# Performance work log

Measured on AMD Instinct MI355X. Metric: run time of the kernel, lower is better.

## Reference

```python
import jax, jax.numpy as jnp
import numpy as np

N_NODES = 20000
N_EDGES = 320000
N_INPUT = 128
N_HIDDEN = 128
N_LAYERS = 3
N_OUT = 2
C_WEIGHT = 1.0
BN_EPS = 1e-5


def _psi(z):
    # sign(z) * log(1 + |z|), the LorentzNet scalar map
    return jnp.sign(z) * jnp.log1p(jnp.abs(z))


def _mink_dot(a, b):
    # Minkowski inner product, metric diag(+1, -1, ..., -1)
    return a[:, 0] * b[:, 0] - jnp.sum(a[:, 1:] * b[:, 1:], axis=1)


def setup_inputs() -> dict:
    key = jax.random.key(0)
    ks = jax.random.split(key, 12)
    n, h, L = N_INPUT, N_HIDDEN, N_LAYERS
    d_in = 2 * n + 6
    f32 = jnp.float32
    inp = {
        "x": jax.random.normal(ks[0], (N_NODES, n), f32),
        "edge_index": jax.random.randint(ks[1], (2, N_EDGES), 0, N_NODES),
        "edge_attr": jax.random.normal(ks[2], (N_EDGES, 4), f32),
        # phi_e: Linear(d_in->h, no bias), BN(h), ReLU, Linear(h->h), ReLU
        "W1": (jax.random.normal(ks[3], (L, d_in, h), f32) / np.sqrt(d_in)).astype(f32),
        "gamma": jnp.ones((L, h), f32),
        "beta": jnp.zeros((L, h), f32),
        "W2": (jax.random.normal(ks[4], (L, h, h), f32) / np.sqrt(h)).astype(f32),
        "b2": jnp.zeros((L, h), f32),
        # phi_x: Linear(h->h), ReLU, Linear(h->1, no bias, xavier gain 1e-3)
        "Wa": (jax.random.normal(ks[5], (L, h, h), f32) / np.sqrt(h)).astype(f32),
        "ba": jnp.zeros((L, h), f32),
        "Wb": (jax.random.normal(ks[6], (L, h, 1), f32) * 1e-3).astype(f32),
        # phi_m: Linear(h->1), Sigmoid
        "Wm": (jax.random.normal(ks[7], (L, h, 1), f32) / np.sqrt(h)).astype(f32),
        "bm": jnp.zeros((L, 1), f32),
        # final edge_mlp: Linear(h -> N_OUT)
        "We": (jax.random.normal(ks[8], (h, N_OUT), f32) / np.sqrt(h)).astype(f32),
        "be": jnp.zeros((N_OUT,), f32),
    }
    return inp


def _lgeb_layer(x, row, col, edge_attr, W1, gamma, beta, W2, b2, Wa, ba, Wb, Wm, bm):
    x_i = x[row]                       # [E, n] gather (aggregation target)
    x_j = x[col]                       # [E, n]
    x_diff = x_i - x_j                 # [E, n]
    norms = _psi(_mink_dot(x_diff, x_diff))[:, None]   # [E, 1]
    dots = _psi(_mink_dot(x_i, x_j))[:, None]          # [E, 1]
    m = jnp.concatenate([x_i, x_j, edge_attr, norms, dots], axis=1)  # [E, 2n+6]
    # phi_e
    hpre = m @ W1                                       # [E, h]
    mu = jnp.mean(hpre, axis=0)
    var = jnp.mean(jnp.square(hpre - mu), axis=0)       # biased, torch BN train mode
    hbn = (hpre - mu) * jax.lax.rsqrt(var + BN_EPS) * gamma + beta
    hid = jax.nn.relu(hbn)
    m_ij = jax.nn.relu(hid @ W2 + b2)                   # [E, h]
    # phi_m gate
    w = jax.nn.sigmoid(m_ij @ Wm + bm)                  # [E, 1]
    m_ij = m_ij * w
    # phi_x scalar weight on x_diff
    s = jax.nn.relu(m_ij @ Wa + ba) @ Wb                # [E, 1]
    trans = jnp.clip(x_diff * s, -100.0, 100.0)         # [E, n]
    x_agg = jax.ops.segment_sum(trans, row, num_segments=x.shape[0])  # [N, n]
    return x + C_WEIGHT * x_agg


def reference(x, edge_index, edge_attr, W1, gamma, beta, W2, b2,
              Wa, ba, Wb, Wm, bm, We, be):
    row, col = edge_index[0], edge_index[1]
    for l in range(N_LAYERS):
        x = _lgeb_layer(x, row, col, edge_attr,
                        W1[l], gamma[l], beta[l], W2[l], b2[l],
                        Wa[l], ba[l], Wb[l], Wm[l], bm[l])
    return jax.nn.sigmoid(x @ We + be)                  # [N, N_OUT]


if __name__ == "__main__":
    out = reference(**setup_inputs())
    print(out.shape, out.dtype)
```

## Files before the change

kernel.cpp:

```cpp
#include <hip/hip_runtime.h>
#include <math.h>

#define NND 20000
#define NE  320000
#define NF  128
#define EPS 1e-5f
#define TE  64
#define NT  256
#define NTILES (NE / TE)
#define NGRP (NE / 4)
#define XST 136
#define BST 40

typedef short short8 __attribute__((ext_vector_type(8)));
typedef float float4v __attribute__((ext_vector_type(4)));

__device__ __forceinline__ float psif(float z) {
    return copysignf(log1pf(fabsf(z)), z);
}
__device__ __forceinline__ float sigm(float z) {
    return 1.f / (1.f + expf(-z));
}
__device__ __forceinline__ short f2bf(float f) {
    union { float f; unsigned u; } v; v.f = f;
    unsigned r = v.u + 0x7fffu + ((v.u >> 16) & 1u);
    return (short)(r >> 16);
}
__device__ __forceinline__ float bf2f(short u) {
    union { unsigned u; float f; } v; v.u = ((unsigned)(unsigned short)u) << 16;
    return v.f;
}
__device__ __forceinline__ float clipf(float v) {
    return fminf(fmaxf(v, -100.f), 100.f);
}

__device__ __forceinline__ void stage_b(const unsigned short* __restrict__ wsrc, int wstride,
                                        int ks, short* bt, int t) {
    #pragma unroll
    for (int rr = 0; rr < 2; ++rr) {
        int c = t + rr * 256;
        int n = c >> 2, h = c & 3;
        short8 v = *(const short8*)(wsrc + (size_t)n * wstride + ks * 32 + h * 8);
        *(short8*)(bt + n * BST + h * 8) = v;
    }
}

__device__ __forceinline__ void ldreg_b(const unsigned short* __restrict__ w, int wstride,
                                        int ks, int t, short8* r) {
    #pragma unroll
    for (int rr = 0; rr < 2; ++rr) {
        int c = t + rr * 256;
        int n = c >> 2, h = c & 3;
        r[rr] = *(const short8*)(w + (size_t)n * wstride + ks * 32 + h * 8);
    }
}
__device__ __forceinline__ void wrlds_b(short* bt, int t, const short8* r) {
    #pragma unroll
    for (int rr = 0; rr < 2; ++rr) {
        int c = t + rr * 256;
        int n = c >> 2, h = c & 3;
        *(short8*)(bt + n * BST + h * 8) = r[rr];
    }
}

__global__ __launch_bounds__(NT, 2)
void node_gemm(const float* __restrict__ x,
               const unsigned short* __restrict__ wt,
               float* __restrict__ PQ,
               float* __restrict__ gstats)
{
    __shared__ short lxa[TE * XST];
    __shared__ short lbt[128 * BST];

    const int t = threadIdx.x;
    const int lane = t & 63, quad = lane >> 4, ln15 = lane & 15;
    const int wv = t >> 6, we = wv >> 1, wc = wv & 1;
    const int n0 = blockIdx.x * 64;
    const int ch = blockIdx.y;
    const unsigned short* wsrc = wt + (size_t)ch * 128 * 128;

    if (blockIdx.x == 0 && ch == 0) gstats[t] = 0.f;

    {
        int row = t >> 2, q = t & 3;
        int src = min(n0 + row, NND - 1);
        const float4* xp = (const float4*)(x + (size_t)src * NF) + q * 8;
        #pragma unroll
        for (int u = 0; u < 4; ++u) {
            float4 a = xp[2*u], b = xp[2*u+1];
            short8 s;
            s[0]=f2bf(a.x); s[1]=f2bf(a.y); s[2]=f2bf(a.z); s[3]=f2bf(a.w);
            s[4]=f2bf(b.x); s[5]=f2bf(b.y); s[6]=f2bf(b.z); s[7]=f2bf(b.w);
            *(short8*)(lxa + row * XST + q * 32 + u * 8) = s;
        }
    }

    float4v acc[2][4];
    #pragma unroll
    for (int a = 0; a < 2; ++a)
        #pragma unroll
        for (int b = 0; b < 4; ++b) { float4v z = {0.f,0.f,0.f,0.f}; acc[a][b] = z; }

    for (int ks = 0; ks < 4; ++ks) {
        __syncthreads();
        stage_b(wsrc, NF, ks, lbt, t);
        __syncthreads();
        short8 af[2], bfr[4];
        #pragma unroll
        for (int ef = 0; ef < 2; ++ef)
            af[ef] = *(const short8*)(lxa + (we*32 + ef*16 + ln15) * XST + ks*32 + quad*8);
        #pragma unroll
        for (int fc = 0; fc < 4; ++fc)
            bfr[fc] = *(const short8*)(lbt + (wc*64 + fc*16 + ln15) * BST + quad*8);
        #pragma unroll
        for (int ef = 0; ef < 2; ++ef)
            #pragma unroll
            for (int fc = 0; fc < 4; ++fc)
                acc[ef][fc] = __builtin_amdgcn_mfma_f32_16x16x32_bf16(af[ef], bfr[fc], acc[ef][fc], 0, 0, 0);
    }
    #pragma unroll
    for (int fc = 0; fc < 4; ++fc) {
        int c = wc * 64 + fc * 16 + ln15;
        #pragma unroll
        for (int ef = 0; ef < 2; ++ef)
            #pragma unroll
            for (int rg = 0; rg < 4; ++rg) {
                int nrow = n0 + we * 32 + ef * 16 + quad * 4 + rg;
                if (nrow < NND)
                    PQ[(size_t)nrow * 256 + ch * 128 + c] = acc[ef][fc][rg];
            }
    }
}

__global__ __launch_bounds__(NT, 4)
void edge_pass(const float* __restrict__ x,
               const float* __restrict__ PQ,
               const int* __restrict__ rowS,
               const int* __restrict__ colS,
               const float* __restrict__ eaS,
               const float* __restrict__ W1l,
               unsigned short* __restrict__ hpre,
               float* __restrict__ gstats)
{
    __shared__ float sred[4][256];

    const int t = threadIdx.x;
    const int lane = t & 63;
    const int wv = t >> 6;
    const int gg = lane >> 4;
    const int ln15 = lane & 15;
    const int c0 = ln15 * 8;

    float w6[6][8];
    #pragma unroll
    for (int k = 0; k < 6; ++k) {
        const float4* wp = (const float4*)(W1l + (size_t)(256 + k) * NF + c0);
        float4 a = wp[0], b = wp[1];
        w6[k][0] = a.x; w6[k][1] = a.y; w6[k][2] = a.z; w6[k][3] = a.w;
        w6[k][4] = b.x; w6[k][5] = b.y; w6[k][6] = b.z; w6[k][7] = b.w;
    }

    float ss[8], sq[8];
    #pragma unroll
    for (int i = 0; i < 8; ++i) { ss[i] = 0.f; sq[i] = 0.f; }

    const int wid = blockIdx.x * 4 + wv;
    const int nw  = gridDim.x * 4;

    for (int g = wid; g < NGRP; g += nw) {
        const int e = g * 4 + gg;
        const int r = rowS[e];
        const int c = colS[e];
        const float4* xip = (const float4*)(x  + (size_t)r * NF  + c0);
        const float4* xjp = (const float4*)(x  + (size_t)c * NF  + c0);
        const float4* prp = (const float4*)(PQ + (size_t)r * 256 + c0);
        const float4* pcp = (const float4*)(PQ + (size_t)c * 256 + 128 + c0);
        float4 xi0 = xip[0], xi1 = xip[1];
        float4 xj0 = xjp[0], xj1 = xjp[1];
        float4 pr0 = prp[0], pr1 = prp[1];
        float4 pc0 = pcp[0], pc1 = pcp[1];
        float4 ea  = ((const float4*)eaS)[e];

        float xiv[8] = {xi0.x, xi0.y, xi0.z, xi0.w, xi1.x, xi1.y, xi1.z, xi1.w};
        float xjv[8] = {xj0.x, xj0.y, xj0.z, xj0.w, xj1.x, xj1.y, xj1.z, xj1.w};

        float nrm = 0.f, dot = 0.f;
        #pragma unroll
        for (int i = 0; i < 8; ++i) {
            float d = xiv[i] - xjv[i];
            nrm = fmaf(-d, d, nrm);
            dot = fmaf(-xiv[i], xjv[i], dot);
        }
        if (ln15 == 0) {
            float d0 = xiv[0] - xjv[0];
            nrm += 2.f * d0 * d0;
            dot += 2.f * xiv[0] * xjv[0];
        }
        nrm += __shfl_xor(nrm, 1); nrm += __shfl_xor(nrm, 2);
        nrm += __shfl_xor(nrm, 4); nrm += __shfl_xor(nrm, 8);
        dot += __shfl_xor(dot, 1); dot += __shfl_xor(dot, 2);
        dot += __shfl_xor(dot, 4); dot += __shfl_xor(dot, 8);
        const float pn = psif(nrm), pd = psif(dot);

        float prv[8] = {pr0.x, pr0.y, pr0.z, pr0.w, pr1.x, pr1.y, pr1.z, pr1.w};
        float pcv[8] = {pc0.x, pc0.y, pc0.z, pc0.w, pc1.x, pc1.y, pc1.z, pc1.w};

        short8 o;
        #pragma unroll
        for (int i = 0; i < 8; ++i) {
            float v = prv[i] + pcv[i];
            v = fmaf(ea.x, w6[0][i], v);
            v = fmaf(ea.y, w6[1][i], v);
            v = fmaf(ea.z, w6[2][i], v);
            v = fmaf(ea.w, w6[3][i], v);
            v = fmaf(pn,   w6[4][i], v);
            v = fmaf(pd,   w6[5][i], v);
            ss[i] += v;
            sq[i] = fmaf(v, v, sq[i]);
            o[i] = f2bf(v);
        }
        *(short8*)(hpre + (size_t)e * NF + c0) = o;
    }

    #pragma unroll
    for (int i = 0; i < 8; ++i) {
        ss[i] += __shfl_xor(ss[i], 16); ss[i] += __shfl_xor(ss[i], 32);
        sq[i] += __shfl_xor(sq[i], 16); sq[i] += __shfl_xor(sq[i], 32);
    }
    if (lane < 16) {
        #pragma unroll
        for (int i = 0; i < 8; ++i) {
            sred[wv][c0 + i]       = ss[i];
            sred[wv][128 + c0 + i] = sq[i];
        }
    }
    __syncthreads();
    atomicAdd(&gstats[t], sred[0][t] + sred[1][t] + sred[2][t] + sred[3][t]);
}

__global__ __launch_bounds__(NT, 4)
void passB(const unsigned short* __restrict__ hpre,
           const float* __restrict__ gstats,
           const float* __restrict__ gamma,
           const float* __restrict__ beta,
           const unsigned short* __restrict__ wt2,
           const float* __restrict__ b2,
           const unsigned short* __restrict__ wta,
           const float* __restrict__ ba,
           const float* __restrict__ wb,
           const float* __restrict__ wm,
           const float* __restrict__ bm,
           float* __restrict__ sG)
{
    __shared__ short lxi[TE * XST];
    __shared__ short lbt0[128 * BST];
    __shared__ short lbt1[128 * BST];
    __shared__ float gpart[2][TE];
    __shared__ float spart[2][TE];
    __shared__ float wgt[TE];
    __shared__ float scs[NF], sfs[NF];

    const int t = threadIdx.x;
    const int lane = t & 63, quad = lane >> 4, ln15 = lane & 15;
    const int wv = t >> 6, we = wv >> 1, wc = wv & 1;
    const int e0 = blockIdx.x * TE;
    const float bmv = bm[0];

    if (t < NF) {
        float mu  = gstats[t] * (1.f / NE);
        float var = fmaxf(gstats[128 + t] * (1.f / NE) - mu * mu, 0.f);
        float inv = rsqrtf(var + EPS);
        float sc  = gamma[t] * inv;
        scs[t] = sc;
        sfs[t] = beta[t] - mu * sc;
    }
    __syncthreads();

    {
        const int le = t >> 2, q = t & 3;
        const unsigned short* hp = hpre + (size_t)(e0 + le) * NF + q * 32;
        #pragma unroll
        for (int h = 0; h < 4; ++h) {
            short8 v = *(const short8*)(hp + h * 8);
            short o[8];
            #pragma unroll
            for (int i = 0; i < 8; ++i) {
                int chn = q * 32 + h * 8 + i;
                float f = fmaxf(fmaf(bf2f(v[i]), scs[chn], sfs[chn]), 0.f);
                o[i] = f2bf(f);
            }
            *(short8*)(lxi + le * XST + q * 32 + h * 8) = *(short8*)o;
        }
    }

    float4v acc[2][4];
    #pragma unroll
    for (int a = 0; a < 2; ++a)
        #pragma unroll
        for (int b = 0; b < 4; ++b) { float4v z = {0.f,0.f,0.f,0.f}; acc[a][b] = z; }

    {
        short8 pre[2];
        ldreg_b(wt2, NF, 0, t, pre);
        wrlds_b(lbt0, t, pre);
        __syncthreads();
        for (int ks = 0; ks < 4; ++ks) {
            short8 nxt[2];
            if (ks < 3) ldreg_b(wt2, NF, ks + 1, t, nxt);
            const short* cur = (ks & 1) ? lbt1 : lbt0;
            short8 af[2], bfr[4];
            #pragma unroll
            for (int ef = 0; ef < 2; ++ef)
                af[ef] = *(const short8*)(lxi + (we*32 + ef*16 + ln15) * XST + ks*32 + quad*8);
            #pragma unroll
            for (int fc = 0; fc < 4; ++fc)
                bfr[fc] = *(const short8*)(cur + (wc*64 + fc*16 + ln15) * BST + quad*8);
            #pragma unroll
            for (int ef = 0; ef < 2; ++ef)
                #pragma unroll
                for (int fc = 0; fc < 4; ++fc)
                    acc[ef][fc] = __builtin_amdgcn_mfma_f32_16x16x32_bf16(af[ef], bfr[fc], acc[ef][fc], 0, 0, 0);
            if (ks < 3) wrlds_b((ks & 1) ? lbt0 : lbt1, t, nxt);
            __syncthreads();
        }
    }

    {
        float p[2][4] = {{0.f,0.f,0.f,0.f},{0.f,0.f,0.f,0.f}};
        #pragma unroll
        for (int fc = 0; fc < 4; ++fc) {
            int c = wc * 64 + fc * 16 + ln15;
            float bb = b2[c], wmv = wm[c];
            #pragma unroll
            for (int ef = 0; ef < 2; ++ef)
                #pragma unroll
                for (int rg = 0; rg < 4; ++rg) {
                    int r = we * 32 + ef * 16 + quad * 4 + rg;
                    float v = fmaxf(acc[ef][fc][rg] + bb, 0.f);
                    lxi[r * XST + c] = f2bf(v);
                    p[ef][rg] = fmaf(v, wmv, p[ef][rg]);
                }
        }
        #pragma unroll
        for (int ef = 0; ef < 2; ++ef)
            #pragma unroll
            for (int rg = 0; rg < 4; ++rg) {
                p[ef][rg] += __shfl_xor(p[ef][rg], 1);
                p[ef][rg] += __shfl_xor(p[ef][rg], 2);
                p[ef][rg] += __shfl_xor(p[ef][rg], 4);
                p[ef][rg] += __shfl_xor(p[ef][rg], 8);
            }
        if (ln15 == 0) {
            #pragma unroll
            for (int ef = 0; ef < 2; ++ef)
                #pragma unroll
                for (int rg = 0; rg < 4; ++rg)
                    gpart[wc][we * 32 + ef * 16 + quad * 4 + rg] = p[ef][rg];
        }
    }

    #pragma unroll
    for (int a = 0; a < 2; ++a)
        #pragma unroll
        for (int b = 0; b < 4; ++b) { float4v z = {0.f,0.f,0.f,0.f}; acc[a][b] = z; }
    {
        short8 pre[2];
        ldreg_b(wta, NF, 0, t, pre);
        wrlds_b(lbt0, t, pre);
        __syncthreads();
        if (t < TE) wgt[t] = sigm(gpart[0][t] + gpart[1][t] + bmv);
        for (int ks = 0; ks < 4; ++ks) {
            short8 nxt[2];
            if (ks < 3) ldreg_b(wta, NF, ks + 1, t, nxt);
            const short* cur = (ks & 1) ? lbt1 : lbt0;
            short8 af[2], bfr[4];
            #pragma unroll
            for (int ef = 0; ef < 2; ++ef)
                af[ef] = *(const short8*)(lxi + (we*32 + ef*16 + ln15) * XST + ks*32 + quad*8);
            #pragma unroll
            for (int fc = 0; fc < 4; ++fc)
                bfr[fc] = *(const short8*)(cur + (wc*64 + fc*16 + ln15) * BST + quad*8);
            #pragma unroll
            for (int ef = 0; ef < 2; ++ef)
                #pragma unroll
                for (int fc = 0; fc < 4; ++fc)
                    acc[ef][fc] = __builtin_amdgcn_mfma_f32_16x16x32_bf16(af[ef], bfr[fc], acc[ef][fc], 0, 0, 0);
            if (ks < 3) wrlds_b((ks & 1) ? lbt0 : lbt1, t, nxt);
            __syncthreads();
        }
    }
    {
        float p[2][4] = {{0.f,0.f,0.f,0.f},{0.f,0.f,0.f,0.f}};
        #pragma unroll
        for (int fc = 0; fc < 4; ++fc) {
            int c = wc * 64 + fc * 16 + ln15;
            float bav = ba[c], wbv = wb[c];
            #pragma unroll
            for (int ef = 0; ef < 2; ++ef)
                #pragma unroll
                for (int rg = 0; rg < 4; ++rg) {
                    int r = we * 32 + ef * 16 + quad * 4 + rg;
                    float v = fmaxf(fmaf(wgt[r], acc[ef][fc][rg], bav), 0.f);
                    p[ef][rg] = fmaf(v, wbv, p[ef][rg]);
                }
        }
        #pragma unroll
        for (int ef = 0; ef < 2; ++ef)
            #pragma unroll
            for (int rg = 0; rg < 4; ++rg) {
                p[ef][rg] += __shfl_xor(p[ef][rg], 1);
                p[ef][rg] += __shfl_xor(p[ef][rg], 2);
                p[ef][rg] += __shfl_xor(p[ef][rg], 4);
                p[ef][rg] += __shfl_xor(p[ef][rg], 8);
            }
        if (ln15 == 0) {
            #pragma unroll
            for (int ef = 0; ef < 2; ++ef)
                #pragma unroll
                for (int rg = 0; rg < 4; ++rg)
                    spart[wc][we * 32 + ef * 16 + quad * 4 + rg] = p[ef][rg];
        }
    }
    __syncthreads();
    if (t < TE) sG[e0 + t] = spart[0][t] + spart[1][t];
}

__global__ __launch_bounds__(NT)
void hist_k(const int* __restrict__ ei, int* __restrict__ deg)
{
    int e = blockIdx.x * NT + threadIdx.x;
    if (e < NE) atomicAdd(&deg[ei[e]], 1);
}

__global__ __launch_bounds__(NT)
void scan_k(const int* __restrict__ deg, int* __restrict__ rowstart,
            int* __restrict__ cursor)
{
    __shared__ int part[NT];
    const int t = threadIdx.x;
    const int CH = (NND + NT - 1) / NT;
    const int base = t * CH;
    int sum = 0;
    for (int i = 0; i < CH; ++i) {
        int idx = base + i;
        if (idx < NND) sum += deg[idx];
    }
    part[t] = sum;
    __syncthreads();
    int pre = 0;
    for (int j = 0; j < t; ++j) pre += part[j];
    int run = pre;
    for (int i = 0; i < CH; ++i) {
        int idx = base + i;
        if (idx < NND) {
            rowstart[idx] = run;
            cursor[idx]   = run;
            run += deg[idx];
        }
    }
    if (t == NT - 1) rowstart[NND] = run;
}

__global__ __launch_bounds__(NT)
void fill_k(const int* __restrict__ ei, int* __restrict__ cursor,
            int* __restrict__ perm)
{
    int e = blockIdx.x * NT + threadIdx.x;
    if (e < NE) {
        int pos = atomicAdd(&cursor[ei[e]], 1);
        perm[pos] = e;
    }
}

__global__ __launch_bounds__(NT)
void prep_edges(const int* __restrict__ ei, const float* __restrict__ eattr,
                const int* __restrict__ perm,
                int* __restrict__ rowS, int* __restrict__ colS,
                float* __restrict__ eaS)
{
    int p = blockIdx.x * NT + threadIdx.x;
    if (p >= NE) return;
    int e = perm[p];
    rowS[p] = ei[e];
    colS[p] = ei[NE + e];
    ((float4*)eaS)[p] = ((const float4*)eattr)[e];
}

__global__ __launch_bounds__(NT)
void aggregate_k(const float* __restrict__ x,
                 const float* __restrict__ sG,
                 const int* __restrict__ rowstart,
                 const int* __restrict__ colS,
                 float* __restrict__ xn)
{
    const int w  = (blockIdx.x * NT + threadIdx.x) >> 6;
    const int ln = threadIdx.x & 63;
    if (w >= NND) return;
    const int beg = rowstart[w], end = rowstart[w + 1];
    const float* xr = x + (size_t)w * NF;
    const float xr0 = xr[ln], xr1 = xr[ln + 64];
    float a0 = 0.f, a1 = 0.f;
    int p = beg;
    if (p < end) {
        int c = colS[p];
        float v0 = x[(size_t)c * NF + ln];
        float v1 = x[(size_t)c * NF + 64 + ln];
        for (; p + 1 < end; ++p) {
            int c2 = colS[p + 1];
            float w0 = x[(size_t)c2 * NF + ln];
            float w1 = x[(size_t)c2 * NF + 64 + ln];
            float s = sG[p];
            a0 += clipf((xr0 - v0) * s);
            a1 += clipf((xr1 - v1) * s);
            v0 = w0; v1 = w1;
        }
        float s = sG[p];
        a0 += clipf((xr0 - v0) * s);
        a1 += clipf((xr1 - v1) * s);
    }
    xn[(size_t)w * NF + ln]      = xr0 + a0;
    xn[(size_t)w * NF + ln + 64] = xr1 + a1;
}

__global__ __launch_bounds__(NT)
void aggregate_final(const float* __restrict__ x,
                     const float* __restrict__ sG,
                     const int* __restrict__ rowstart,
                     const int* __restrict__ colS,
                     const float* __restrict__ We,
                     const float* __restrict__ be,
                     float* __restrict__ out)
{
    const int w  = (blockIdx.x * NT + threadIdx.x) >> 6;
    const int ln = threadIdx.x & 63;
    if (w >= NND) return;
    const int beg = rowstart[w], end = rowstart[w + 1];
    const float* xr = x + (size_t)w * NF;
    const float xr0 = xr[ln], xr1 = xr[ln + 64];
    float a0 = 0.f, a1 = 0.f;
    int p = beg;
    if (p < end) {
        int c = colS[p];
        float v0 = x[(size_t)c * NF + ln];
        float v1 = x[(size_t)c * NF + 64 + ln];
        for (; p + 1 < end; ++p) {
            int c2 = colS[p + 1];
            float w0 = x[(size_t)c2 * NF + ln];
            float w1 = x[(size_t)c2 * NF + 64 + ln];
            float s = sG[p];
            a0 += clipf((xr0 - v0) * s);
            a1 += clipf((xr1 - v1) * s);
            v0 = w0; v1 = w1;
        }
        float s = sG[p];
        a0 += clipf((xr0 - v0) * s);
        a1 += clipf((xr1 - v1) * s);
    }
    const float v0 = xr0 + a0;
    const float v1 = xr1 + a1;
    float o0 = v0 * We[ln * 2]     + v1 * We[(ln + 64) * 2];
    float o1 = v0 * We[ln * 2 + 1] + v1 * We[(ln + 64) * 2 + 1];
    #pragma unroll
    for (int m = 1; m < 64; m <<= 1) { o0 += __shfl_xor(o0, m); o1 += __shfl_xor(o1, m); }
    if (ln == 0) {
        out[w * 2]     = sigm(o0 + be[0]);
        out[w * 2 + 1] = sigm(o1 + be[1]);
    }
}

__global__ __launch_bounds__(NT)
void prep_w1n(const float* __restrict__ W1, unsigned short* __restrict__ wt)
{
    int i = blockIdx.x * NT + threadIdx.x;
    if (i >= 3 * 256 * 128) return;
    int l = i / (256 * 128);
    int r = i % (256 * 128);
    int cc = r / 128, k = r % 128;
    int srow = (cc < 128) ? k : 128 + k;
    int scol = (cc < 128) ? cc : cc - 128;
    wt[i] = (unsigned short)f2bf(W1[((size_t)l * 262 + srow) * 128 + scol]);
}

__global__ __launch_bounds__(NT)
void prep_w128(const float* __restrict__ W, unsigned short* __restrict__ wt)
{
    int i = blockIdx.x * NT + threadIdx.x;
    if (i >= 3 * 128 * 128) return;
    int l = i / (128 * 128);
    int r = i % (128 * 128);
    int n = r / 128, k = r % 128;
    wt[i] = (unsigned short)f2bf(W[((size_t)l * 128 + k) * 128 + n]);
}

extern "C" void kernel_launch(void* const* d_in, const int* in_sizes, int n_in,
                              void* d_out, int out_size, void* d_ws, size_t ws_size,
                              hipStream_t stream) {
    const float* x   = (const float*)d_in[0];
    const int*   ei  = (const int*)d_in[1];
    const float* ea  = (const float*)d_in[2];
    const float* W1  = (const float*)d_in[3];
    const float* ga  = (const float*)d_in[4];
    const float* bet = (const float*)d_in[5];
    const float* W2  = (const float*)d_in[6];
    const float* b2  = (const float*)d_in[7];
    const float* Wa  = (const float*)d_in[8];
    const float* ba  = (const float*)d_in[9];
    const float* Wb  = (const float*)d_in[10];
    const float* Wm  = (const float*)d_in[11];
    const float* bm  = (const float*)d_in[12];
    const float* We  = (const float*)d_in[13];
    const float* be  = (const float*)d_in[14];
    float* out = (float*)d_out;

    char* base = (char*)d_ws;
    size_t off = 0;
    auto alloc = [&](size_t bytes) -> void* {
        off = (off + 31) & ~(size_t)31;
        void* p = base + off;
        off += bytes;
        return p;
    };
    float* gstats   = (float*)alloc(256 * sizeof(float));
    int*   deg      = (int*)alloc(NND * sizeof(int));
    int*   rowstart = (int*)alloc((NND + 1) * sizeof(int));
    int*   cursor   = (int*)alloc(NND * sizeof(int));
    int*   perm     = (int*)alloc(NE * sizeof(int));
    int*   rowS     = (int*)alloc(NE * sizeof(int));
    int*   colS     = (int*)alloc(NE * sizeof(int));
    float* eaS      = (float*)alloc((size_t)NE * 4 * sizeof(float));
    float* sG       = (float*)alloc(NE * sizeof(float));
    float* xA       = (float*)alloc((size_t)NND * NF * sizeof(float));
    float* xB       = (float*)alloc((size_t)NND * NF * sizeof(float));
    float* PQ       = (float*)alloc((size_t)NND * 256 * sizeof(float));
    unsigned short* wt1n = (unsigned short*)alloc((size_t)3 * 256 * 128 * 2);
    unsigned short* wt2  = (unsigned short*)alloc((size_t)3 * 128 * 128 * 2);
    unsigned short* wta  = (unsigned short*)alloc((size_t)3 * 128 * 128 * 2);
    unsigned short* hpreG= (unsigned short*)alloc((size_t)NE * NF * 2);

    prep_w1n <<<(3 * 256 * 128 + NT - 1) / NT, NT, 0, stream>>>(W1, wt1n);
    prep_w128<<<(3 * 128 * 128 + NT - 1) / NT, NT, 0, stream>>>(W2, wt2);
    prep_w128<<<(3 * 128 * 128 + NT - 1) / NT, NT, 0, stream>>>(Wa, wta);

    hipMemsetAsync(deg, 0, NND * sizeof(int), stream);
    hist_k<<<(NE + NT - 1) / NT, NT, 0, stream>>>(ei, deg);
    scan_k<<<1, NT, 0, stream>>>(deg, rowstart, cursor);
    fill_k<<<(NE + NT - 1) / NT, NT, 0, stream>>>(ei, cursor, perm);
    prep_edges<<<(NE + NT - 1) / NT, NT, 0, stream>>>(ei, ea, perm, rowS, colS, eaS);

    const float* xc = x;
    float* buf[2] = { xA, xB };

    for (int l = 0; l < 3; ++l) {
        node_gemm<<<dim3((NND + 63) / 64, 2), NT, 0, stream>>>(
            xc, wt1n + (size_t)l * 256 * 128, PQ, gstats);
        edge_pass<<<1024, NT, 0, stream>>>(xc, PQ, rowS, colS, eaS,
                                           W1 + (size_t)l * 262 * 128, hpreG, gstats);
        passB<<<NTILES, NT, 0, stream>>>(hpreG, gstats, ga + l * NF, bet + l * NF,
                                         wt2 + (size_t)l * 128 * 128, b2 + l * NF,
                                         wta + (size_t)l * 128 * 128, ba + l * NF,
                                         Wb + l * NF, Wm + l * NF, bm + l, sG);
        if (l < 2) {
            float* xn = buf[l & 1];
            aggregate_k<<<(NND * 64 + NT - 1) / NT, NT, 0, stream>>>(xc, sG, rowstart,
                                                                     colS, xn);
            xc = xn;
        } else {
            aggregate_final<<<(NND * 64 + NT - 1) / NT, NT, 0, stream>>>(xc, sG, rowstart,
                                                                         colS, We, be, out);
        }
    }
}
```

Measured before the change: 740.7 us.

## Pack bf16 x_j and Q_j into one record for the random-column gather

The column-side gathers in edge_pass (x_j and the Q half of the node GEMM) are moved out of two fp32 arrays into a single packed bf16 record per node. node_gemm writes Q as bf16 into this record, while aggregate_k and a new pack_x kernel write bf16 copies of x. This halves the bytes of the scattered col gather and keeps each node's data on contiguous cache lines. The cost is extra writes, one more kernel and bf16 rounding of x_j in the norm/dot and pre-activation sums. The edge_pass grid is also doubled.

```diff
diff --git a/kernel.cpp b/kernel.cpp
--- a/kernel.cpp
+++ b/kernel.cpp
@@ -66,7 +66,8 @@
 __global__ __launch_bounds__(NT, 2)
 void node_gemm(const float* __restrict__ x,
                const unsigned short* __restrict__ wt,
-               float* __restrict__ PQ,
+               float* __restrict__ P,
+               unsigned short* __restrict__ rec,
                float* __restrict__ gstats)
 {
     __shared__ short lxa[TE * XST];
@@ -126,15 +127,35 @@
             #pragma unroll
             for (int rg = 0; rg < 4; ++rg) {
                 int nrow = n0 + we * 32 + ef * 16 + quad * 4 + rg;
-                if (nrow < NND)
-                    PQ[(size_t)nrow * 256 + ch * 128 + c] = acc[ef][fc][rg];
+                if (nrow < NND) {
+                    if (ch == 0)
+                        P[(size_t)nrow * NF + c] = acc[ef][fc][rg];
+                    else
+                        rec[(size_t)nrow * 256 + 128 + c] =
+                            (unsigned short)f2bf(acc[ef][fc][rg]);
+                }
             }
     }
+}
+
+__global__ __launch_bounds__(NT)
+void pack_x(const float* __restrict__ x, unsigned short* __restrict__ rec)
+{
+    int i = blockIdx.x * NT + threadIdx.x;
+    if (i >= NND * 16) return;
+    int n = i >> 4, q = i & 15;
+    const float4* xp = (const float4*)(x + (size_t)n * NF + q * 8);
+    float4 a = xp[0], b = xp[1];
+    short8 s;
+    s[0]=f2bf(a.x); s[1]=f2bf(a.y); s[2]=f2bf(a.z); s[3]=f2bf(a.w);
+    s[4]=f2bf(b.x); s[5]=f2bf(b.y); s[6]=f2bf(b.z); s[7]=f2bf(b.w);
+    *(short8*)(rec + (size_t)n * 256 + q * 8) = s;
 }
 
 __global__ __launch_bounds__(NT, 4)
 void edge_pass(const float* __restrict__ x,
-               const float* __restrict__ PQ,
+               const float* __restrict__ P,
+               const unsigned short* __restrict__ rec,
                const int* __restrict__ rowS,
                const int* __restrict__ colS,
                const float* __restrict__ eaS,
@@ -171,18 +192,18 @@
         const int e = g * 4 + gg;
         const int r = rowS[e];
         const int c = colS[e];
-        const float4* xip = (const float4*)(x  + (size_t)r * NF  + c0);
-        const float4* xjp = (const float4*)(x  + (size_t)c * NF  + c0);
-        const float4* prp = (const float4*)(PQ + (size_t)r * 256 + c0);
-        const float4* pcp = (const float4*)(PQ + (size_t)c * 256 + 128 + c0);
+        const float4* xip = (const float4*)(x + (size_t)r * NF + c0);
+        const float4* prp = (const float4*)(P + (size_t)r * NF + c0);
+        short8 xjb = *(const short8*)(rec + (size_t)c * 256 + c0);
+        short8 qjb = *(const short8*)(rec + (size_t)c * 256 + 128 + c0);
         float4 xi0 = xip[0], xi1 = xip[1];
-        float4 xj0 = xjp[0], xj1 = xjp[1];
         float4 pr0 = prp[0], pr1 = prp[1];
-        float4 pc0 = pcp[0], pc1 = pcp[1];
         float4 ea  = ((const float4*)eaS)[e];
 
         float xiv[8] = {xi0.x, xi0.y, xi0.z, xi0.w, xi1.x, xi1.y, xi1.z, xi1.w};
-        float xjv[8] = {xj0.x, xj0.y, xj0.z, xj0.w, xj1.x, xj1.y, xj1.z, xj1.w};
+        float xjv[8];
+        #pragma unroll
+        for (int i = 0; i < 8; ++i) xjv[i] = bf2f(xjb[i]);
 
         float nrm = 0.f, dot = 0.f;
         #pragma unroll
@@ -203,12 +224,11 @@
         const float pn = psif(nrm), pd = psif(dot);
 
         float prv[8] = {pr0.x, pr0.y, pr0.z, pr0.w, pr1.x, pr1.y, pr1.z, pr1.w};
-        float pcv[8] = {pc0.x, pc0.y, pc0.z, pc0.w, pc1.x, pc1.y, pc1.z, pc1.w};
 
         short8 o;
         #pragma unroll
         for (int i = 0; i < 8; ++i) {
-            float v = prv[i] + pcv[i];
+            float v = prv[i] + bf2f(qjb[i]);
             v = fmaf(ea.x, w6[0][i], v);
             v = fmaf(ea.y, w6[1][i], v);
             v = fmaf(ea.z, w6[2][i], v);
@@ -491,7 +511,8 @@
                  const float* __restrict__ sG,
                  const int* __restrict__ rowstart,
                  const int* __restrict__ colS,
-                 float* __restrict__ xn)
+                 float* __restrict__ xn,
+                 unsigned short* __restrict__ rec)
 {
     const int w  = (blockIdx.x * NT + threadIdx.x) >> 6;
     const int ln = threadIdx.x & 63;
@@ -518,8 +539,12 @@
         a0 += clipf((xr0 - v0) * s);
         a1 += clipf((xr1 - v1) * s);
     }
-    xn[(size_t)w * NF + ln]      = xr0 + a0;
-    xn[(size_t)w * NF + ln + 64] = xr1 + a1;
+    const float o0 = xr0 + a0;
+    const float o1 = xr1 + a1;
+    xn[(size_t)w * NF + ln]      = o0;
+    xn[(size_t)w * NF + ln + 64] = o1;
+    rec[(size_t)w * 256 + ln]      = (unsigned short)f2bf(o0);
+    rec[(size_t)w * 256 + 64 + ln] = (unsigned short)f2bf(o1);
 }
 
 __global__ __launch_bounds__(NT)
@@ -631,7 +656,8 @@
     float* sG       = (float*)alloc(NE * sizeof(float));
     float* xA       = (float*)alloc((size_t)NND * NF * sizeof(float));
     float* xB       = (float*)alloc((size_t)NND * NF * sizeof(float));
-    float* PQ       = (float*)alloc((size_t)NND * 256 * sizeof(float));
+    float* P        = (float*)alloc((size_t)NND * NF * sizeof(float));
+    unsigned short* rec  = (unsigned short*)alloc((size_t)NND * 256 * 2);
     unsigned short* wt1n = (unsigned short*)alloc((size_t)3 * 256 * 128 * 2);
     unsigned short* wt2  = (unsigned short*)alloc((size_t)3 * 128 * 128 * 2);
     unsigned short* wta  = (unsigned short*)alloc((size_t)3 * 128 * 128 * 2);
@@ -646,14 +672,15 @@
     scan_k<<<1, NT, 0, stream>>>(deg, rowstart, cursor);
     fill_k<<<(NE + NT - 1) / NT, NT, 0, stream>>>(ei, cursor, perm);
     prep_edges<<<(NE + NT - 1) / NT, NT, 0, stream>>>(ei, ea, perm, rowS, colS, eaS);
+    pack_x<<<(NND * 16 + NT - 1) / NT, NT, 0, stream>>>(x, rec);
 
     const float* xc = x;
     float* buf[2] = { xA, xB };
 
     for (int l = 0; l < 3; ++l) {
         node_gemm<<<dim3((NND + 63) / 64, 2), NT, 0, stream>>>(
-            xc, wt1n + (size_t)l * 256 * 128, PQ, gstats);
-        edge_pass<<<1024, NT, 0, stream>>>(xc, PQ, rowS, colS, eaS,
+            xc, wt1n + (size_t)l * 256 * 128, P, rec, gstats);
+        edge_pass<<<2048, NT, 0, stream>>>(xc, P, rec, rowS, colS, eaS,
                                            W1 + (size_t)l * 262 * 128, hpreG, gstats);
         passB<<<NTILES, NT, 0, stream>>>(hpreG, gstats, ga + l * NF, bet + l * NF,
                                          wt2 + (size_t)l * 128 * 128, b2 + l * NF,
@@ -662,7 +689,7 @@
         if (l < 2) {
             float* xn = buf[l & 1];
             aggregate_k<<<(NND * 64 + NT - 1) / NT, NT, 0, stream>>>(xc, sG, rowstart,
-                                                                     colS, xn);
+                                                                     colS, xn, rec);
             xc = xn;
         } else {
             aggregate_final<<<(NND * 64 + NT - 1) / NT, NT, 0, stream>>>(xc, sG, rowstart,
```

New measurement: 749.2 us. No clear change (+1.1%).
